# Performance work log

Measured on AMD Instinct MI355X. Metric: run time of the kernel, lower is better.

The kernel has to match this reference:

```python
import jax, jax.numpy as jnp
import numpy as np

N = 50000   # residue nodes
E = 800000  # edges per edge type
T = 3       # edge types
L = 3       # conv layers (len(hidden_channels)-1)
IN, H, ENC, OUT, K = 64, 128, 100, 32, 128
COMMIT = 0.25
EPS = 1e-5


def gelu(x):
    return jax.nn.gelu(x, approximate=False)  # torch nn.GELU default (erf)


def setup_inputs() -> dict:
    key = jax.random.key(0)
    ks = iter(jax.random.split(key, 40))
    p = lambda shp, s=0.05: jax.random.normal(next(ks), shp, jnp.float32) * s
    inp = {
        'x_res': p((N, IN), 1.0),
        'x_AA': p((N, 20), 1.0),
        'edge_index': jax.random.randint(next(ks), (T, 2, E), 0, N, jnp.int32),
        # input block
        'ln_gamma': jnp.ones((IN,), jnp.float32),
        'ln_beta': jnp.zeros((IN,), jnp.float32),
        'W1': p((IN, 2 * H)), 'b1': jnp.zeros((2 * H,), jnp.float32),
        'W2': p((2 * H, H)), 'b2': jnp.zeros((H,), jnp.float32),
        # body: SAGE convs, [layer, edge_type, ...]
        'sage_Wl': p((L, T, H, H)),  # applied to aggregated neighbors
        'sage_Wr': p((L, T, H, H)),  # applied to root
        'sage_b': jnp.zeros((L, T, H), jnp.float32),
        # GraphNorm per layer
        'gn_weight': jnp.ones((L, H), jnp.float32),
        'gn_bias': jnp.zeros((L, H), jnp.float32),
        'gn_scale': jnp.ones((L, H), jnp.float32),  # mean_scale
        # head
        'Wh1': p((H * L, ENC)), 'bh1': jnp.zeros((ENC,), jnp.float32),
        'Wh2': p((ENC, ENC)), 'bh2': jnp.zeros((ENC,), jnp.float32),
        'Wo1': p((ENC + 20, ENC)), 'bo1': jnp.zeros((ENC,), jnp.float32),
        'Wo2': p((ENC, ENC)), 'bo2': jnp.zeros((ENC,), jnp.float32),
        'Wo3': p((ENC, OUT)), 'bo3': jnp.zeros((OUT,), jnp.float32),
        # VQ codebook
        'codebook': p((K, OUT), 0.5),
    }
    return inp


def _sage(x, src, dst, Wl, Wr, b):
    # SAGEConv, mean aggregation: out = Wl @ mean_{src->dst}(x[src]) + Wr @ x + b
    msg = x[src]                                             # [E, H] gather
    s = jax.ops.segment_sum(msg, dst, num_segments=N)        # [N, H] scatter-add
    cnt = jax.ops.segment_sum(jnp.ones((msg.shape[0],), x.dtype), dst, num_segments=N)
    agg = s / jnp.maximum(cnt, 1.0)[:, None]
    return agg @ Wl + x @ Wr + b


def _graphnorm(x, weight, bias, scale):
    # PyG GraphNorm over a single graph
    out = x - scale * x.mean(0)
    var = (out * out).mean(0)
    return out * jax.lax.rsqrt(var + EPS) * weight + bias


def reference(x_res, x_AA, edge_index, ln_gamma, ln_beta, W1, b1, W2, b2,
              sage_Wl, sage_Wr, sage_b, gn_weight, gn_bias, gn_scale,
              Wh1, bh1, Wh2, bh2, Wo1, bo1, Wo2, bo2, Wo3, bo3, codebook):
    # input: LayerNorm + (dropout = identity in eval) + inmlp
    mu = x_res.mean(-1, keepdims=True)
    var = x_res.var(-1, keepdims=True)
    xr = (x_res - mu) * jax.lax.rsqrt(var + EPS) * ln_gamma + ln_beta
    x = gelu(gelu(xr @ W1 + b1) @ W2 + b2)                   # [N, H]

    # body: per-edge-type SAGE conv -> stack-mean -> GELU -> GraphNorm; JK cat
    x_save = []
    for i in range(L):
        xs = [_sage(x, edge_index[t, 0], edge_index[t, 1],
                    sage_Wl[i, t], sage_Wr[i, t], sage_b[i, t]) for t in range(T)]
        x = jnp.mean(jnp.stack(xs, 0), 0)
        x = gelu(x)
        x = _graphnorm(x, gn_weight[i], gn_bias[i], gn_scale[i])
        x_save.append(x)
    x = jnp.concatenate(x_save, axis=1)                      # [N, H*L] JumpingKnowledge cat

    # head
    x = gelu(gelu(x @ Wh1 + bh1) @ Wh2 + bh2)
    x = jnp.concatenate([x, x_AA], axis=1)
    x = gelu(x @ Wo1 + bo1)
    x = gelu(x @ Wo2 + bo2)
    x = jnp.tanh(x @ Wo3 + bo3)                              # [N, OUT]

    # VectorQuantizer (straight-through)
    d = (jnp.sum(x * x, 1, keepdims=True)
         - 2.0 * x @ codebook.T
         + jnp.sum(codebook * codebook, 1)[None, :])         # [N, K]
    idx = jnp.argmin(d, axis=1)
    q = codebook[idx]                                        # [N, OUT]
    e_latent = jnp.mean((jax.lax.stop_gradient(q) - x) ** 2)
    q_latent = jnp.mean((q - jax.lax.stop_gradient(x)) ** 2)
    vq_loss = q_latent + COMMIT * e_latent
    z_q = x + jax.lax.stop_gradient(q - x)
    return z_q, vq_loss
```

## Files before the change

### kernel.cpp

```cpp
#include <hip/hip_runtime.h>

#define N_ 50000
#define E_ 800000
#define T_ 3
#define NG_ (T_ * N_)
#define EPS_ 1e-5f

__device__ __forceinline__ float gelu_f(float x) {
    return 0.5f * x * (1.0f + erff(x * 0.70710678118654752440f));
}

__global__ void k_prep(const float* __restrict__ Wl, const float* __restrict__ Wr,
                       const float* __restrict__ b, float* wls, float* wra, float* ba) {
    int i = blockIdx.x * 256 + threadIdx.x;
    const float third = 1.0f / 3.0f;
    if (i < 9 * 128 * 128) wls[i] = Wl[i] * third;
    if (i < 3 * 128 * 128) {
        int l = i >> 14, rem = i & 16383;
        const float* p = Wr + l * 3 * 16384 + rem;
        wra[i] = (p[0] + p[16384] + p[32768]) * third;
    }
    if (i < 3 * 128) {
        int l = i >> 7, c = i & 127;
        const float* p = b + l * 3 * 128 + c;
        ba[i] = (p[0] + p[128] + p[256]) * third;
    }
}

__global__ void k_link(const int* __restrict__ EI, int* __restrict__ head, int* __restrict__ nxt) {
    int i = blockIdx.x * 256 + threadIdx.x;
    if (i >= T_ * E_) return;
    int t = i / E_, e = i - t * E_;
    int d = EI[(t * 2 + 1) * E_ + e];
    nxt[i] = atomicExch(&head[t * N_ + d], i);
}

__global__ __launch_bounds__(256) void k_compact(
    const int* __restrict__ EI, const int* __restrict__ head, const int* __restrict__ nxt,
    int* __restrict__ cursor, int* __restrict__ cnt, int* __restrict__ rpA,
    float* __restrict__ inv, int* __restrict__ csr) {
    int tid = threadIdx.x;
    int g = blockIdx.x * 256 + tid;
    bool ok = (g < NG_);
    int lane = tid & 63;
    int c = 0;
    int h = -1;
    if (ok) {
        h = head[g];
        int e = h;
        while (e >= 0) { c++; e = nxt[e]; }
        cnt[g] = c;
        inv[g] = 1.0f / (float)(c > 0 ? c : 1);
    }
    int x = c;
    for (int off = 1; off < 64; off <<= 1) {
        int y = __shfl_up(x, off);
        if (lane >= off) x += y;
    }
    int total = __shfl(x, 63);
    int base = 0;
    if (lane == 63 && total > 0) base = atomicAdd(cursor, total);
    base = __shfl(base, 63);
    if (ok) {
        int pos = base + x - c;
        rpA[g] = pos;
        int e = h;
        while (e >= 0) {
            int t = e / E_, idx = e - t * E_;
            csr[pos++] = EI[(t * 2) * E_ + idx];
            e = nxt[e];
        }
    }
}

__global__ __launch_bounds__(256) void k_inmlp(
    const float* __restrict__ xres, const float* __restrict__ gam, const float* __restrict__ bet,
    const float* __restrict__ W1, const float* __restrict__ b1,
    const float* __restrict__ W2, const float* __restrict__ b2, float* __restrict__ x0) {
    __shared__ float xr[32][68];
    __shared__ float h1[32][260];
    int tid = threadIdx.x;
    int base = blockIdx.x * 32;
    for (int i = 0; i < 2; ++i) {
        int f4 = i * 256 + tid;
        int r = f4 >> 4, c4 = f4 & 15;
        float4 v = make_float4(0.f, 0.f, 0.f, 0.f);
        int gr = base + r;
        if (gr < N_) v = *(const float4*)&xres[gr * 64 + c4 * 4];
        *(float4*)&xr[r][c4 * 4] = v;
    }
    __syncthreads();
    if (tid < 32) {
        int r = tid;
        float s = 0.f;
        for (int k = 0; k < 64; ++k) s += xr[r][k];
        float mu = s * (1.0f / 64.0f);
        float v = 0.f;
        for (int k = 0; k < 64; ++k) { float d = xr[r][k] - mu; v += d * d; }
        float rs = rsqrtf(v * (1.0f / 64.0f) + EPS_);
        for (int k = 0; k < 64; ++k)
            xr[r][k] = (xr[r][k] - mu) * rs * gam[k] + bet[k];
    }
    __syncthreads();
    {
        int tx = tid & 63, ty = tid >> 6;
        int c0 = tx * 4, r0 = ty * 8;
        float acc[8][4];
        for (int r = 0; r < 8; ++r)
            for (int j = 0; j < 4; ++j) acc[r][j] = b1[c0 + j];
        for (int k0 = 0; k0 < 64; k0 += 4) {
            float4 a[8], w[4];
            for (int r = 0; r < 8; ++r) a[r] = *(const float4*)&xr[r0 + r][k0];
            for (int kk = 0; kk < 4; ++kk) w[kk] = *(const float4*)&W1[(k0 + kk) * 256 + c0];
            for (int kk = 0; kk < 4; ++kk)
                for (int r = 0; r < 8; ++r) {
                    float as = (&a[r].x)[kk];
                    acc[r][0] = fmaf(as, w[kk].x, acc[r][0]);
                    acc[r][1] = fmaf(as, w[kk].y, acc[r][1]);
                    acc[r][2] = fmaf(as, w[kk].z, acc[r][2]);
                    acc[r][3] = fmaf(as, w[kk].w, acc[r][3]);
                }
        }
        for (int r = 0; r < 8; ++r)
            for (int j = 0; j < 4; ++j) h1[r0 + r][c0 + j] = gelu_f(acc[r][j]);
    }
    __syncthreads();
    {
        int tx = tid & 31, ty = tid >> 5;
        int c0 = tx * 4, r0 = ty * 4;
        float acc[4][4];
        for (int r = 0; r < 4; ++r)
            for (int j = 0; j < 4; ++j) acc[r][j] = b2[c0 + j];
        for (int k0 = 0; k0 < 256; k0 += 4) {
            float4 a[4], w[4];
            for (int r = 0; r < 4; ++r) a[r] = *(const float4*)&h1[r0 + r][k0];
            for (int kk = 0; kk < 4; ++kk) w[kk] = *(const float4*)&W2[(k0 + kk) * 128 + c0];
            for (int kk = 0; kk < 4; ++kk)
                for (int r = 0; r < 4; ++r) {
                    float as = (&a[r].x)[kk];
                    acc[r][0] = fmaf(as, w[kk].x, acc[r][0]);
                    acc[r][1] = fmaf(as, w[kk].y, acc[r][1]);
                    acc[r][2] = fmaf(as, w[kk].z, acc[r][2]);
                    acc[r][3] = fmaf(as, w[kk].w, acc[r][3]);
                }
        }
        for (int r = 0; r < 4; ++r) {
            int gr = base + r0 + r;
            if (gr < N_) {
                float4 v = make_float4(gelu_f(acc[r][0]), gelu_f(acc[r][1]),
                                       gelu_f(acc[r][2]), gelu_f(acc[r][3]));
                *(float4*)&x0[(long)gr * 128 + c0] = v;
            }
        }
    }
}

__global__ __launch_bounds__(256) void k_gather(
    const int* __restrict__ rpA, const int* __restrict__ cnt, const int* __restrict__ csr,
    const float* __restrict__ inv, const float* __restrict__ X, int ldx, float* __restrict__ agg) {
    int tid = threadIdx.x;
    int g = blockIdx.x * 4 + (tid >> 6);
    if (g >= NG_) return;
    int lane = tid & 63;
    int sub = lane >> 4;
    int f = (lane & 15) * 8;
    int start = rpA[g];
    int end = start + cnt[g];
    float4 s0 = make_float4(0.f, 0.f, 0.f, 0.f);
    float4 s1 = make_float4(0.f, 0.f, 0.f, 0.f);
    for (int e = start + sub; e < end; e += 4) {
        int sn = csr[e];
        const float* row = &X[(long)sn * ldx + f];
        const float4 v0 = *(const float4*)row;
        const float4 v1 = *(const float4*)(row + 4);
        s0.x += v0.x; s0.y += v0.y; s0.z += v0.z; s0.w += v0.w;
        s1.x += v1.x; s1.y += v1.y; s1.z += v1.z; s1.w += v1.w;
    }
    s0.x += __shfl_xor(s0.x, 16); s0.y += __shfl_xor(s0.y, 16);
    s0.z += __shfl_xor(s0.z, 16); s0.w += __shfl_xor(s0.w, 16);
    s1.x += __shfl_xor(s1.x, 16); s1.y += __shfl_xor(s1.y, 16);
    s1.z += __shfl_xor(s1.z, 16); s1.w += __shfl_xor(s1.w, 16);
    s0.x += __shfl_xor(s0.x, 32); s0.y += __shfl_xor(s0.y, 32);
    s0.z += __shfl_xor(s0.z, 32); s0.w += __shfl_xor(s0.w, 32);
    s1.x += __shfl_xor(s1.x, 32); s1.y += __shfl_xor(s1.y, 32);
    s1.z += __shfl_xor(s1.z, 32); s1.w += __shfl_xor(s1.w, 32);
    if (sub == 0) {
        float iv = inv[g];
        float* op = &agg[(long)g * 128 + f];
        *(float4*)op = make_float4(s0.x * iv, s0.y * iv, s0.z * iv, s0.w * iv);
        *(float4*)(op + 4) = make_float4(s1.x * iv, s1.y * iv, s1.z * iv, s1.w * iv);
    }
}

__global__ __launch_bounds__(256) void k_gemm_body(
    const float* __restrict__ X, int ldx, const float* __restrict__ agg,
    const float* __restrict__ wls_l, const float* __restrict__ wra_l, const float* __restrict__ ba_l,
    float* __restrict__ g_out, float* __restrict__ cs_l, float* __restrict__ cq_l) {
    __shared__ float xs[64][132];
    __shared__ float sd[8][128];
    __shared__ float sq[8][128];
    int tid = threadIdx.x;
    int base = blockIdx.x * 64;
    int tx = tid & 31, ty = tid >> 5;
    int c0 = tx * 4, r0 = ty * 8;
    float acc[8][4];
    for (int r = 0; r < 8; ++r)
        for (int j = 0; j < 4; ++j) acc[r][j] = ba_l[c0 + j];
    for (int seg = 0; seg < 4; ++seg) {
        const float* src; long ld;
        if (seg < 3) { src = agg + ((long)seg * N_ + base) * 128; ld = 128; }
        else         { src = X + (long)base * ldx; ld = ldx; }
        __syncthreads();
        for (int i = 0; i < 8; ++i) {
            int f4 = i * 256 + tid;
            int r = f4 >> 5, c4 = f4 & 31;
            float4 v = make_float4(0.f, 0.f, 0.f, 0.f);
            if (base + r < N_) v = *(const float4*)&src[(long)r * ld + c4 * 4];
            *(float4*)&xs[r][c4 * 4] = v;
        }
        __syncthreads();
        const float* W = (seg < 3) ? (wls_l + seg * 16384) : wra_l;
        for (int k0 = 0; k0 < 128; k0 += 4) {
            float4 a[8], w[4];
            for (int r = 0; r < 8; ++r) a[r] = *(const float4*)&xs[r0 + r][k0];
            for (int kk = 0; kk < 4; ++kk) w[kk] = *(const float4*)&W[(k0 + kk) * 128 + c0];
            for (int kk = 0; kk < 4; ++kk)
                for (int r = 0; r < 8; ++r) {
                    float as = (&a[r].x)[kk];
                    acc[r][0] = fmaf(as, w[kk].x, acc[r][0]);
                    acc[r][1] = fmaf(as, w[kk].y, acc[r][1]);
                    acc[r][2] = fmaf(as, w[kk].z, acc[r][2]);
                    acc[r][3] = fmaf(as, w[kk].w, acc[r][3]);
                }
        }
    }
    float csum[4] = {0.f, 0.f, 0.f, 0.f};
    float qsum[4] = {0.f, 0.f, 0.f, 0.f};
    for (int r = 0; r < 8; ++r) {
        int gr = base + r0 + r;
        if (gr < N_) {
            float g0 = gelu_f(acc[r][0]), g1 = gelu_f(acc[r][1]);
            float g2 = gelu_f(acc[r][2]), g3 = gelu_f(acc[r][3]);
            *(float4*)&g_out[(long)gr * 128 + c0] = make_float4(g0, g1, g2, g3);
            csum[0] += g0; csum[1] += g1; csum[2] += g2; csum[3] += g3;
            qsum[0] += g0 * g0; qsum[1] += g1 * g1; qsum[2] += g2 * g2; qsum[3] += g3 * g3;
        }
    }
    *(float4*)&sd[ty][c0] = make_float4(csum[0], csum[1], csum[2], csum[3]);
    *(float4*)&sq[ty][c0] = make_float4(qsum[0], qsum[1], qsum[2], qsum[3]);
    __syncthreads();
    if (tid < 128) {
        float t = 0.f, q = 0.f;
        for (int i = 0; i < 8; ++i) { t += sd[i][tid]; q += sq[i][tid]; }
        atomicAdd(&cs_l[tid], t);
        atomicAdd(&cq_l[tid], q);
    }
}

__global__ __launch_bounds__(256) void k_pass3(const float* __restrict__ g,
                                               const float* __restrict__ cs_l, const float* __restrict__ cq_l,
                                               const float* __restrict__ gsc,
                                               const float* __restrict__ gw, const float* __restrict__ gb,
                                               float* __restrict__ xs_l) {
    int tid = threadIdx.x;
    int c = tid & 127, half = tid >> 7;
    int base = blockIdx.x * 128 + half * 64;
    float mu = cs_l[c] / 50000.0f;
    float sm = gsc[c] * mu;
    float var = cq_l[c] / 50000.0f - 2.0f * sm * mu + sm * sm;
    float mul = rsqrtf(var + EPS_) * gw[c];
    float add = gb[c];
    for (int i = 0; i < 64; ++i) {
        int r = base + i;
        if (r < N_) xs_l[(long)r * 384 + c] = (g[(long)r * 128 + c] - sm) * mul + add;
    }
}

__global__ __launch_bounds__(256) void k_head1(const float* __restrict__ xsave,
    const float* __restrict__ Wh1, const float* __restrict__ bh1,
    const float* __restrict__ Wh2, const float* __restrict__ bh2,
    float* __restrict__ h2out) {
    __shared__ float at[64][68];
    __shared__ float h1b[64][104];
    int tid = threadIdx.x;
    int base = blockIdx.x * 64;
    int tx = tid & 31, ty = tid >> 5;
    int c0 = tx * 4, r0 = ty * 8;
    bool valid = (c0 < 100);
    float acc[8][4];
    for (int r = 0; r < 8; ++r)
        for (int j = 0; j < 4; ++j) acc[r][j] = valid ? bh1[c0 + j] : 0.f;
    for (int kt = 0; kt < 6; ++kt) {
        __syncthreads();
        for (int i = 0; i < 4; ++i) {
            int f4 = i * 256 + tid;
            int r = f4 >> 4, c4 = f4 & 15;
            float4 v = make_float4(0.f, 0.f, 0.f, 0.f);
            int gr = base + r;
            if (gr < N_) v = *(const float4*)&xsave[(long)gr * 384 + kt * 64 + c4 * 4];
            *(float4*)&at[r][c4 * 4] = v;
        }
        __syncthreads();
        if (valid) {
            for (int k0 = 0; k0 < 64; k0 += 4) {
                float4 a[8], w[4];
                for (int r = 0; r < 8; ++r) a[r] = *(const float4*)&at[r0 + r][k0];
                for (int kk = 0; kk < 4; ++kk) w[kk] = *(const float4*)&Wh1[(kt * 64 + k0 + kk) * 100 + c0];
                for (int kk = 0; kk < 4; ++kk)
                    for (int r = 0; r < 8; ++r) {
                        float as = (&a[r].x)[kk];
                        acc[r][0] = fmaf(as, w[kk].x, acc[r][0]);
                        acc[r][1] = fmaf(as, w[kk].y, acc[r][1]);
                        acc[r][2] = fmaf(as, w[kk].z, acc[r][2]);
                        acc[r][3] = fmaf(as, w[kk].w, acc[r][3]);
                    }
            }
        }
    }
    __syncthreads();
    if (valid)
        for (int r = 0; r < 8; ++r)
            for (int j = 0; j < 4; ++j) h1b[r0 + r][c0 + j] = gelu_f(acc[r][j]);
    __syncthreads();
    {
        float acc2[8][4];
        for (int r = 0; r < 8; ++r)
            for (int j = 0; j < 4; ++j) acc2[r][j] = valid ? bh2[c0 + j] : 0.f;
        if (valid) {
            for (int k0 = 0; k0 < 100; k0 += 4) {
                float4 a[8], w[4];
                for (int r = 0; r < 8; ++r) a[r] = *(const float4*)&h1b[r0 + r][k0];
                for (int kk = 0; kk < 4; ++kk) w[kk] = *(const float4*)&Wh2[(k0 + kk) * 100 + c0];
                for (int kk = 0; kk < 4; ++kk)
                    for (int r = 0; r < 8; ++r) {
                        float as = (&a[r].x)[kk];
                        acc2[r][0] = fmaf(as, w[kk].x, acc2[r][0]);
                        acc2[r][1] = fmaf(as, w[kk].y, acc2[r][1]);
                        acc2[r][2] = fmaf(as, w[kk].z, acc2[r][2]);
                        acc2[r][3] = fmaf(as, w[kk].w, acc2[r][3]);
                    }
            }
            for (int r = 0; r < 8; ++r) {
                int gr = base + r0 + r;
                if (gr < N_) {
                    float4 v = make_float4(gelu_f(acc2[r][0]), gelu_f(acc2[r][1]),
                                           gelu_f(acc2[r][2]), gelu_f(acc2[r][3]));
                    *(float4*)&h2out[(long)gr * 100 + c0] = v;
                }
            }
        }
    }
}

__global__ __launch_bounds__(256) void k_head2a(const float* __restrict__ h2,
    const float* __restrict__ xAA,
    const float* __restrict__ Wo1, const float* __restrict__ bo1,
    const float* __restrict__ Wo2, const float* __restrict__ bo2,
    const float* __restrict__ Wo3, const float* __restrict__ bo3,
    float* __restrict__ xf) {
    __shared__ float A[64][124];
    __shared__ float B[64][104];
    int tid = threadIdx.x;
    int base = blockIdx.x * 64;
    for (int i = 0; i < 7; ++i) {
        int f4 = i * 256 + tid;
        if (f4 < 1600) {
            int r = f4 / 25, c4 = f4 - r * 25;
            float4 v = make_float4(0.f, 0.f, 0.f, 0.f);
            int gr = base + r;
            if (gr < N_) v = *(const float4*)&h2[(long)gr * 100 + c4 * 4];
            *(float4*)&A[r][c4 * 4] = v;
        }
    }
    for (int i = 0; i < 2; ++i) {
        int f4 = i * 256 + tid;
        if (f4 < 320) {
            int r = f4 / 5, c4 = f4 - r * 5;
            float4 v = make_float4(0.f, 0.f, 0.f, 0.f);
            int gr = base + r;
            if (gr < N_) v = *(const float4*)&xAA[(long)gr * 20 + c4 * 4];
            *(float4*)&A[r][100 + c4 * 4] = v;
        }
    }
    __syncthreads();
    int tx = tid & 31, ty = tid >> 5;
    int c0 = tx * 4, r0 = ty * 8;
    bool valid = (c0 < 100);
    {
        float acc[8][4];
        for (int r = 0; r < 8; ++r)
            for (int j = 0; j < 4; ++j) acc[r][j] = valid ? bo1[c0 + j] : 0.f;
        if (valid) {
            for (int k0 = 0; k0 < 120; k0 += 4) {
                float4 a[8], w[4];
                for (int r = 0; r < 8; ++r) a[r] = *(const float4*)&A[r0 + r][k0];
                for (int kk = 0; kk < 4; ++kk) w[kk] = *(const float4*)&Wo1[(k0 + kk) * 100 + c0];
                for (int kk = 0; kk < 4; ++kk)
                    for (int r = 0; r < 8; ++r) {
                        float as = (&a[r].x)[kk];
                        acc[r][0] = fmaf(as, w[kk].x, acc[r][0]);
                        acc[r][1] = fmaf(as, w[kk].y, acc[r][1]);
                        acc[r][2] = fmaf(as, w[kk].z, acc[r][2]);
                        acc[r][3] = fmaf(as, w[kk].w, acc[r][3]);
                    }
            }
            for (int r = 0; r < 8; ++r)
                for (int j = 0; j < 4; ++j) B[r0 + r][c0 + j] = gelu_f(acc[r][j]);
        }
    }
    __syncthreads();
    {
        float acc[8][4];
        for (int r = 0; r < 8; ++r)
            for (int j = 0; j < 4; ++j) acc[r][j] = valid ? bo2[c0 + j] : 0.f;
        if (valid) {
            for (int k0 = 0; k0 < 100; k0 += 4) {
                float4 a[8], w[4];
                for (int r = 0; r < 8; ++r) a[r] = *(const float4*)&B[r0 + r][k0];
                for (int kk = 0; kk < 4; ++kk) w[kk] = *(const float4*)&Wo2[(k0 + kk) * 100 + c0];
                for (int kk = 0; kk < 4; ++kk)
                    for (int r = 0; r < 8; ++r) {
                        float as = (&a[r].x)[kk];
                        acc[r][0] = fmaf(as, w[kk].x, acc[r][0]);
                        acc[r][1] = fmaf(as, w[kk].y, acc[r][1]);
                        acc[r][2] = fmaf(as, w[kk].z, acc[r][2]);
                        acc[r][3] = fmaf(as, w[kk].w, acc[r][3]);
                    }
            }
        }
        __syncthreads();
        if (valid)
            for (int r = 0; r < 8; ++r)
                for (int j = 0; j < 4; ++j) A[r0 + r][c0 + j] = gelu_f(acc[r][j]);
    }
    __syncthreads();
    {
        int c0b = (tid & 7) * 4, rg = tid >> 3;
        int r0b = rg * 2;
        float acc[2][4];
        for (int r = 0; r < 2; ++r)
            for (int j = 0; j < 4; ++j) acc[r][j] = bo3[c0b + j];
        for (int k0 = 0; k0 < 100; k0 += 4) {
            float4 a[2], w[4];
            for (int r = 0; r < 2; ++r) a[r] = *(const float4*)&A[r0b + r][k0];
            for (int kk = 0; kk < 4; ++kk) w[kk] = *(const float4*)&Wo3[(k0 + kk) * 32 + c0b];
            for (int kk = 0; kk < 4; ++kk)
                for (int r = 0; r < 2; ++r) {
                    float as = (&a[r].x)[kk];
                    acc[r][0] = fmaf(as, w[kk].x, acc[r][0]);
                    acc[r][1] = fmaf(as, w[kk].y, acc[r][1]);
                    acc[r][2] = fmaf(as, w[kk].z, acc[r][2]);
                    acc[r][3] = fmaf(as, w[kk].w, acc[r][3]);
                }
        }
        for (int r = 0; r < 2; ++r) {
            int gr = base + r0b + r;
            if (gr < N_) {
                float4 v = make_float4(tanhf(acc[r][0]), tanhf(acc[r][1]),
                                       tanhf(acc[r][2]), tanhf(acc[r][3]));
                *(float4*)&xf[(long)gr * 32 + c0b] = v;
            }
        }
    }
}

__global__ __launch_bounds__(256) void k_vq(const float* __restrict__ xf,
    const float* __restrict__ cb, float* __restrict__ zq, float* __restrict__ loss) {
    __shared__ float CB[128 * 32];
    __shared__ float CC[128];
    __shared__ float SR[256];
    int tid = threadIdx.x;
    for (int i = 0; i < 4; ++i) {
        int f4 = i * 256 + tid;
        *(float4*)&CB[f4 * 4] = *(const float4*)&cb[f4 * 4];
    }
    __syncthreads();
    if (tid < 128) {
        float s = 0.f;
        for (int j = 0; j < 32; ++j) { float v = CB[tid * 32 + j]; s += v * v; }
        CC[tid] = s;
    }
    __syncthreads();
    int node = blockIdx.x * 256 + tid;
    float part = 0.f;
    if (node < N_) {
        float4 xv[8];
        for (int j4 = 0; j4 < 8; ++j4) xv[j4] = *(const float4*)&xf[(long)node * 32 + j4 * 4];
        float xx = 0.f;
        for (int j4 = 0; j4 < 8; ++j4)
            xx += xv[j4].x * xv[j4].x + xv[j4].y * xv[j4].y + xv[j4].z * xv[j4].z + xv[j4].w * xv[j4].w;
        float best = 3.4e38f;
        int bidx = 0;
        for (int k = 0; k < 128; ++k) {
            const float* cbr = &CB[k * 32];
            float dot = 0.f;
            for (int j4 = 0; j4 < 8; ++j4) {
                float4 cv = *(const float4*)&cbr[j4 * 4];
                dot += cv.x * xv[j4].x + cv.y * xv[j4].y + cv.z * xv[j4].z + cv.w * xv[j4].w;
            }
            float d = fmaf(-2.0f, dot, xx) + CC[k];
            if (d < best) { best = d; bidx = k; }
        }
        const float* q = &CB[bidx * 32];
        for (int j4 = 0; j4 < 8; ++j4) {
            float4 qv = *(const float4*)&q[j4 * 4];
            *(float4*)&zq[(long)node * 32 + j4 * 4] = qv;
            float4 xvv = xv[j4];
            float d0 = qv.x - xvv.x, d1 = qv.y - xvv.y, d2 = qv.z - xvv.z, d3 = qv.w - xvv.w;
            part += d0 * d0 + d1 * d1 + d2 * d2 + d3 * d3;
        }
    }
    SR[tid] = part;
    __syncthreads();
    for (int off = 128; off > 0; off >>= 1) {
        if (tid < off) SR[tid] += SR[tid + off];
        __syncthreads();
    }
    if (tid == 0) atomicAdd(loss, SR[0]);
}

__global__ void k_fin(float* dout, const float* loss) {
    if (threadIdx.x == 0 && blockIdx.x == 0)
        dout[(long)N_ * 32] = 1.25f * (loss[0] / 1600000.0f);
}

extern "C" void kernel_launch(void* const* d_in, const int* in_sizes, int n_in,
                              void* d_out, int out_size, void* d_ws, size_t ws_size,
                              hipStream_t stream) {
    const float* x_res = (const float*)d_in[0];
    const float* x_AA  = (const float*)d_in[1];
    const int*   EI    = (const int*)d_in[2];
    const float* ln_g  = (const float*)d_in[3];
    const float* ln_b  = (const float*)d_in[4];
    const float* W1    = (const float*)d_in[5];
    const float* b1    = (const float*)d_in[6];
    const float* W2    = (const float*)d_in[7];
    const float* b2    = (const float*)d_in[8];
    const float* sWl   = (const float*)d_in[9];
    const float* sWr   = (const float*)d_in[10];
    const float* sb    = (const float*)d_in[11];
    const float* gnw   = (const float*)d_in[12];
    const float* gnb   = (const float*)d_in[13];
    const float* gns   = (const float*)d_in[14];
    const float* Wh1   = (const float*)d_in[15];
    const float* bh1   = (const float*)d_in[16];
    const float* Wh2   = (const float*)d_in[17];
    const float* bh2   = (const float*)d_in[18];
    const float* Wo1   = (const float*)d_in[19];
    const float* bo1   = (const float*)d_in[20];
    const float* Wo2   = (const float*)d_in[21];
    const float* bo2   = (const float*)d_in[22];
    const float* Wo3   = (const float*)d_in[23];
    const float* bo3   = (const float*)d_in[24];
    const float* cbk   = (const float*)d_in[25];
    float* out = (float*)d_out;

    float* ws    = (float*)d_ws;
    float* xsave = ws;
    float* x0    = xsave + (size_t)N_ * 384;
    float* agg   = x0 + (size_t)N_ * 128;
    float* gbuf  = agg + (size_t)3 * N_ * 128;
    float* wls   = gbuf + (size_t)N_ * 128;
    float* wra   = wls + 147456;
    float* ba    = wra + 49152;
    int*   cursor = (int*)(ba + 384);
    float* loss  = (float*)(cursor + 1);
    float* cs    = loss + 1;
    float* cq    = cs + 384;
    int*   head  = (int*)(cq + 384);
    int*   nxt   = head + NG_;
    int*   cnt   = nxt + (size_t)T_ * E_;
    int*   rpA   = cnt + NG_;
    float* inv   = (float*)(rpA + NG_);
    int*   csr   = (int*)(inv + NG_);
    float* h2    = agg + (size_t)N_ * 128;
    float* xf    = gbuf;

    hipMemsetAsync(cursor, 0, 770 * sizeof(int), stream);
    hipMemsetAsync(head, 0xFF, NG_ * sizeof(int), stream);

    k_prep<<<576, 256, 0, stream>>>(sWl, sWr, sb, wls, wra, ba);
    k_link<<<(T_ * E_ + 255) / 256, 256, 0, stream>>>(EI, head, nxt);
    k_compact<<<(NG_ + 255) / 256, 256, 0, stream>>>(EI, head, nxt, cursor, cnt, rpA, inv, csr);
    k_inmlp<<<(N_ + 31) / 32, 256, 0, stream>>>(x_res, ln_g, ln_b, W1, b1, W2, b2, x0);

    for (int l = 0; l < 3; ++l) {
        const float* X = (l == 0) ? x0 : (xsave + (size_t)(l - 1) * 128);
        int ldx = (l == 0) ? 128 : 384;
        k_gather<<<NG_ / 4, 256, 0, stream>>>(rpA, cnt, csr, inv, X, ldx, agg);
        k_gemm_body<<<(N_ + 63) / 64, 256, 0, stream>>>(X, ldx, agg,
            wls + (size_t)l * 3 * 16384, wra + (size_t)l * 16384, ba + l * 128,
            gbuf, cs + l * 128, cq + l * 128);
        k_pass3<<<(N_ + 127) / 128, 256, 0, stream>>>(gbuf, cs + l * 128, cq + l * 128,
                                                      gns + l * 128, gnw + l * 128, gnb + l * 128,
                                                      xsave + (size_t)l * 128);
    }
    k_head1<<<(N_ + 63) / 64, 256, 0, stream>>>(xsave, Wh1, bh1, Wh2, bh2, h2);
    k_head2a<<<(N_ + 63) / 64, 256, 0, stream>>>(h2, x_AA, Wo1, bo1, Wo2, bo2, Wo3, bo3, xf);
    k_vq<<<(N_ + 255) / 256, 256, 0, stream>>>(xf, cbk, out, loss);
    k_fin<<<1, 64, 0, stream>>>(out, loss);
}
```

Measured before the change: 1.518 ms.

## Fold GraphNorm affine into consumers and fuse head kernels

GraphNorm is no longer applied in a separate pass over the activations. The body GEMM writes pre-norm GELU output directly into the JK buffer, a tiny kernel computes per-channel scale and shift, and the next layer's gather, root load and the head apply that affine on the fly. For the gather, the shift is added only when a node has at least one incoming edge, which keeps the mean aggregation correct. The two head kernels are merged into one so the h2 intermediate stays in shared memory, and the input LayerNorm statistics are parallelised across 8 lanes per row. This removes a full read/write pass of N×128 per layer plus an N×100 round trip, at the cost of a few extra FMAs per element in the gather.

```diff
diff --git a/kernel.cpp b/kernel.cpp
--- a/kernel.cpp
+++ b/kernel.cpp
@@ -11,7 +11,8 @@
 }
 
 __global__ void k_prep(const float* __restrict__ Wl, const float* __restrict__ Wr,
-                       const float* __restrict__ b, float* wls, float* wra, float* ba) {
+                       const float* __restrict__ b, float* wls, float* wra, float* ba,
+                       float* idA, float* idB) {
     int i = blockIdx.x * 256 + threadIdx.x;
     const float third = 1.0f / 3.0f;
     if (i < 9 * 128 * 128) wls[i] = Wl[i] * third;
@@ -25,6 +26,7 @@
         const float* p = b + l * 3 * 128 + c;
         ba[i] = (p[0] + p[128] + p[256]) * third;
     }
+    if (i < 128) { idA[i] = 1.0f; idB[i] = 0.0f; }
 }
 
 __global__ void k_link(const int* __restrict__ EI, int* __restrict__ head, int* __restrict__ nxt) {
@@ -90,15 +92,17 @@
         *(float4*)&xr[r][c4 * 4] = v;
     }
     __syncthreads();
-    if (tid < 32) {
-        int r = tid;
+    {
+        int r = tid >> 3, l8 = tid & 7;
         float s = 0.f;
-        for (int k = 0; k < 64; ++k) s += xr[r][k];
+        for (int k = l8; k < 64; k += 8) s += xr[r][k];
+        s += __shfl_xor(s, 1); s += __shfl_xor(s, 2); s += __shfl_xor(s, 4);
         float mu = s * (1.0f / 64.0f);
         float v = 0.f;
-        for (int k = 0; k < 64; ++k) { float d = xr[r][k] - mu; v += d * d; }
+        for (int k = l8; k < 64; k += 8) { float d = xr[r][k] - mu; v += d * d; }
+        v += __shfl_xor(v, 1); v += __shfl_xor(v, 2); v += __shfl_xor(v, 4);
         float rs = rsqrtf(v * (1.0f / 64.0f) + EPS_);
-        for (int k = 0; k < 64; ++k)
+        for (int k = l8; k < 64; k += 8)
             xr[r][k] = (xr[r][k] - mu) * rs * gam[k] + bet[k];
     }
     __syncthreads();
@@ -157,7 +161,8 @@
 
 __global__ __launch_bounds__(256) void k_gather(
     const int* __restrict__ rpA, const int* __restrict__ cnt, const int* __restrict__ csr,
-    const float* __restrict__ inv, const float* __restrict__ X, int ldx, float* __restrict__ agg) {
+    const float* __restrict__ inv, const float* __restrict__ X, int ldx,
+    const float* __restrict__ nA, const float* __restrict__ nB, float* __restrict__ agg) {
     int tid = threadIdx.x;
     int g = blockIdx.x * 4 + (tid >> 6);
     if (g >= NG_) return;
@@ -186,21 +191,35 @@
     s1.z += __shfl_xor(s1.z, 32); s1.w += __shfl_xor(s1.w, 32);
     if (sub == 0) {
         float iv = inv[g];
+        float bsel = (end > start) ? 1.0f : 0.0f;
+        float4 A0 = *(const float4*)&nA[f];
+        float4 A1 = *(const float4*)&nA[f + 4];
+        float4 B0 = *(const float4*)&nB[f];
+        float4 B1 = *(const float4*)&nB[f + 4];
         float* op = &agg[(long)g * 128 + f];
-        *(float4*)op = make_float4(s0.x * iv, s0.y * iv, s0.z * iv, s0.w * iv);
-        *(float4*)(op + 4) = make_float4(s1.x * iv, s1.y * iv, s1.z * iv, s1.w * iv);
+        *(float4*)op = make_float4(fmaf(s0.x * iv, A0.x, bsel * B0.x),
+                                   fmaf(s0.y * iv, A0.y, bsel * B0.y),
+                                   fmaf(s0.z * iv, A0.z, bsel * B0.z),
+                                   fmaf(s0.w * iv, A0.w, bsel * B0.w));
+        *(float4*)(op + 4) = make_float4(fmaf(s1.x * iv, A1.x, bsel * B1.x),
+                                         fmaf(s1.y * iv, A1.y, bsel * B1.y),
+                                         fmaf(s1.z * iv, A1.z, bsel * B1.z),
+                                         fmaf(s1.w * iv, A1.w, bsel * B1.w));
     }
 }
 
 __global__ __launch_bounds__(256) void k_gemm_body(
     const float* __restrict__ X, int ldx, const float* __restrict__ agg,
+    const float* __restrict__ nA, const float* __restrict__ nB,
     const float* __restrict__ wls_l, const float* __restrict__ wra_l, const float* __restrict__ ba_l,
-    float* __restrict__ g_out, float* __restrict__ cs_l, float* __restrict__ cq_l) {
+    float* __restrict__ xsl, float* __restrict__ cs_l, float* __restrict__ cq_l) {
     __shared__ float xs[64][132];
     __shared__ float sd[8][128];
     __shared__ float sq[8][128];
+    __shared__ float nAs[128], nBs[128];
     int tid = threadIdx.x;
     int base = blockIdx.x * 64;
+    if (tid < 128) { nAs[tid] = nA[tid]; nBs[tid] = nB[tid]; }
     int tx = tid & 31, ty = tid >> 5;
     int c0 = tx * 4, r0 = ty * 8;
     float acc[8][4];
@@ -216,6 +235,13 @@
             int r = f4 >> 5, c4 = f4 & 31;
             float4 v = make_float4(0.f, 0.f, 0.f, 0.f);
             if (base + r < N_) v = *(const float4*)&src[(long)r * ld + c4 * 4];
+            if (seg == 3) {
+                int cc = c4 * 4;
+                v.x = fmaf(v.x, nAs[cc], nBs[cc]);
+                v.y = fmaf(v.y, nAs[cc + 1], nBs[cc + 1]);
+                v.z = fmaf(v.z, nAs[cc + 2], nBs[cc + 2]);
+                v.w = fmaf(v.w, nAs[cc + 3], nBs[cc + 3]);
+            }
             *(float4*)&xs[r][c4 * 4] = v;
         }
         __syncthreads();
@@ -241,7 +267,7 @@
         if (gr < N_) {
             float g0 = gelu_f(acc[r][0]), g1 = gelu_f(acc[r][1]);
             float g2 = gelu_f(acc[r][2]), g3 = gelu_f(acc[r][3]);
-            *(float4*)&g_out[(long)gr * 128 + c0] = make_float4(g0, g1, g2, g3);
+            *(float4*)&xsl[(long)gr * 384 + c0] = make_float4(g0, g1, g2, g3);
             csum[0] += g0; csum[1] += g1; csum[2] += g2; csum[3] += g3;
             qsum[0] += g0 * g0; qsum[1] += g1 * g1; qsum[2] += g2 * g2; qsum[3] += g3 * g3;
         }
@@ -257,33 +283,33 @@
     }
 }
 
-__global__ __launch_bounds__(256) void k_pass3(const float* __restrict__ g,
-                                               const float* __restrict__ cs_l, const float* __restrict__ cq_l,
-                                               const float* __restrict__ gsc,
-                                               const float* __restrict__ gw, const float* __restrict__ gb,
-                                               float* __restrict__ xs_l) {
-    int tid = threadIdx.x;
-    int c = tid & 127, half = tid >> 7;
-    int base = blockIdx.x * 128 + half * 64;
+__global__ void k_norm(const float* __restrict__ cs_l, const float* __restrict__ cq_l,
+                       const float* __restrict__ gsc, const float* __restrict__ gw,
+                       const float* __restrict__ gb, float* __restrict__ nA, float* __restrict__ nB) {
+    int c = threadIdx.x;
     float mu = cs_l[c] / 50000.0f;
     float sm = gsc[c] * mu;
     float var = cq_l[c] / 50000.0f - 2.0f * sm * mu + sm * sm;
-    float mul = rsqrtf(var + EPS_) * gw[c];
-    float add = gb[c];
-    for (int i = 0; i < 64; ++i) {
-        int r = base + i;
-        if (r < N_) xs_l[(long)r * 384 + c] = (g[(long)r * 128 + c] - sm) * mul + add;
-    }
-}
-
-__global__ __launch_bounds__(256) void k_head1(const float* __restrict__ xsave,
+    float a = rsqrtf(var + EPS_) * gw[c];
+    nA[c] = a;
+    nB[c] = gb[c] - sm * a;
+}
+
+__global__ __launch_bounds__(256) void k_head(const float* __restrict__ xsave,
+    const float* __restrict__ nA, const float* __restrict__ nB,
     const float* __restrict__ Wh1, const float* __restrict__ bh1,
     const float* __restrict__ Wh2, const float* __restrict__ bh2,
-    float* __restrict__ h2out) {
-    __shared__ float at[64][68];
-    __shared__ float h1b[64][104];
+    const float* __restrict__ xAA,
+    const float* __restrict__ Wo1, const float* __restrict__ bo1,
+    const float* __restrict__ Wo2, const float* __restrict__ bo2,
+    const float* __restrict__ Wo3, const float* __restrict__ bo3,
+    float* __restrict__ xf) {
+    __shared__ __align__(16) float buf0[64 * 124];
+    __shared__ __align__(16) float buf1[64 * 104];
+    __shared__ float nAs[384], nBs[384];
     int tid = threadIdx.x;
     int base = blockIdx.x * 64;
+    for (int i = tid; i < 384; i += 256) { nAs[i] = nA[i]; nBs[i] = nB[i]; }
     int tx = tid & 31, ty = tid >> 5;
     int c0 = tx * 4, r0 = ty * 8;
     bool valid = (c0 < 100);
@@ -295,16 +321,21 @@
         for (int i = 0; i < 4; ++i) {
             int f4 = i * 256 + tid;
             int r = f4 >> 4, c4 = f4 & 15;
+            int col = kt * 64 + c4 * 4;
             float4 v = make_float4(0.f, 0.f, 0.f, 0.f);
             int gr = base + r;
-            if (gr < N_) v = *(const float4*)&xsave[(long)gr * 384 + kt * 64 + c4 * 4];
-            *(float4*)&at[r][c4 * 4] = v;
+            if (gr < N_) v = *(const float4*)&xsave[(long)gr * 384 + col];
+            v.x = fmaf(v.x, nAs[col], nBs[col]);
+            v.y = fmaf(v.y, nAs[col + 1], nBs[col + 1]);
+            v.z = fmaf(v.z, nAs[col + 2], nBs[col + 2]);
+            v.w = fmaf(v.w, nAs[col + 3], nBs[col + 3]);
+            *(float4*)&buf0[r * 68 + c4 * 4] = v;
         }
         __syncthreads();
         if (valid) {
             for (int k0 = 0; k0 < 64; k0 += 4) {
                 float4 a[8], w[4];
-                for (int r = 0; r < 8; ++r) a[r] = *(const float4*)&at[r0 + r][k0];
+                for (int r = 0; r < 8; ++r) a[r] = *(const float4*)&buf0[(r0 + r) * 68 + k0];
                 for (int kk = 0; kk < 4; ++kk) w[kk] = *(const float4*)&Wh1[(kt * 64 + k0 + kk) * 100 + c0];
                 for (int kk = 0; kk < 4; ++kk)
                     for (int r = 0; r < 8; ++r) {
@@ -320,8 +351,18 @@
     __syncthreads();
     if (valid)
         for (int r = 0; r < 8; ++r)
-            for (int j = 0; j < 4; ++j) h1b[r0 + r][c0 + j] = gelu_f(acc[r][j]);
-    __syncthreads();
+            for (int j = 0; j < 4; ++j) buf1[(r0 + r) * 104 + c0 + j] = gelu_f(acc[r][j]);
+    __syncthreads();
+    for (int i = 0; i < 2; ++i) {
+        int f4 = i * 256 + tid;
+        if (f4 < 320) {
+            int r = f4 / 5, c4 = f4 - r * 5;
+            float4 v = make_float4(0.f, 0.f, 0.f, 0.f);
+            int gr = base + r;
+            if (gr < N_) v = *(const float4*)&xAA[(long)gr * 20 + c4 * 4];
+            *(float4*)&buf0[r * 124 + 100 + c4 * 4] = v;
+        }
+    }
     {
         float acc2[8][4];
         for (int r = 0; r < 8; ++r)
@@ -329,7 +370,7 @@
         if (valid) {
             for (int k0 = 0; k0 < 100; k0 += 4) {
                 float4 a[8], w[4];
-                for (int r = 0; r < 8; ++r) a[r] = *(const float4*)&h1b[r0 + r][k0];
+                for (int r = 0; r < 8; ++r) a[r] = *(const float4*)&buf1[(r0 + r) * 104 + k0];
                 for (int kk = 0; kk < 4; ++kk) w[kk] = *(const float4*)&Wh2[(k0 + kk) * 100 + c0];
                 for (int kk = 0; kk < 4; ++kk)
                     for (int r = 0; r < 8; ++r) {
@@ -340,124 +381,85 @@
                         acc2[r][3] = fmaf(as, w[kk].w, acc2[r][3]);
                     }
             }
-            for (int r = 0; r < 8; ++r) {
-                int gr = base + r0 + r;
-                if (gr < N_) {
-                    float4 v = make_float4(gelu_f(acc2[r][0]), gelu_f(acc2[r][1]),
-                                           gelu_f(acc2[r][2]), gelu_f(acc2[r][3]));
-                    *(float4*)&h2out[(long)gr * 100 + c0] = v;
-                }
-            }
-        }
-    }
-}
-
-__global__ __launch_bounds__(256) void k_head2a(const float* __restrict__ h2,
-    const float* __restrict__ xAA,
-    const float* __restrict__ Wo1, const float* __restrict__ bo1,
-    const float* __restrict__ Wo2, const float* __restrict__ bo2,
-    const float* __restrict__ Wo3, const float* __restrict__ bo3,
-    float* __restrict__ xf) {
-    __shared__ float A[64][124];
-    __shared__ float B[64][104];
-    int tid = threadIdx.x;
-    int base = blockIdx.x * 64;
-    for (int i = 0; i < 7; ++i) {
-        int f4 = i * 256 + tid;
-        if (f4 < 1600) {
-            int r = f4 / 25, c4 = f4 - r * 25;
-            float4 v = make_float4(0.f, 0.f, 0.f, 0.f);
-            int gr = base + r;
-            if (gr < N_) v = *(const float4*)&h2[(long)gr * 100 + c4 * 4];
-            *(float4*)&A[r][c4 * 4] = v;
-        }
-    }
-    for (int i = 0; i < 2; ++i) {
-        int f4 = i * 256 + tid;
-        if (f4 < 320) {
-            int r = f4 / 5, c4 = f4 - r * 5;
-            float4 v = make_float4(0.f, 0.f, 0.f, 0.f);
-            int gr = base + r;
-            if (gr < N_) v = *(const float4*)&xAA[(long)gr * 20 + c4 * 4];
-            *(float4*)&A[r][100 + c4 * 4] = v;
-        }
-    }
-    __syncthreads();
-    int tx = tid & 31, ty = tid >> 5;
-    int c0 = tx * 4, r0 = ty * 8;
-    bool valid = (c0 < 100);
+            for (int r = 0; r < 8; ++r)
+                for (int j = 0; j < 4; ++j) buf0[(r0 + r) * 124 + c0 + j] = gelu_f(acc2[r][j]);
+        }
+    }
+    __syncthreads();
     {
-        float acc[8][4];
+        float acc3[8][4];
         for (int r = 0; r < 8; ++r)
-            for (int j = 0; j < 4; ++j) acc[r][j] = valid ? bo1[c0 + j] : 0.f;
+            for (int j = 0; j < 4; ++j) acc3[r][j] = valid ? bo1[c0 + j] : 0.f;
         if (valid) {
             for (int k0 = 0; k0 < 120; k0 += 4) {
                 float4 a[8], w[4];
-                for (int r = 0; r < 8; ++r) a[r] = *(const float4*)&A[r0 + r][k0];
+                for (int r = 0; r < 8; ++r) a[r] = *(const float4*)&buf0[(r0 + r) * 124 + k0];
                 for (int kk = 0; kk < 4; ++kk) w[kk] = *(const float4*)&Wo1[(k0 + kk) * 100 + c0];
                 for (int kk = 0; kk < 4; ++kk)
                     for (int r = 0; r < 8; ++r) {
                         float as = (&a[r].x)[kk];
-                        acc[r][0] = fmaf(as, w[kk].x, acc[r][0]);
-                        acc[r][1] = fmaf(as, w[kk].y, acc[r][1]);
-                        acc[r][2] = fmaf(as, w[kk].z, acc[r][2]);
-                        acc[r][3] = fmaf(as, w[kk].w, acc[r][3]);
+                        acc3[r][0] = fmaf(as, w[kk].x, acc3[r][0]);
+                        acc3[r][1] = fmaf(as, w[kk].y, acc3[r][1]);
+                        acc3[r][2] = fmaf(as, w[kk].z, acc3[r][2]);
+                        acc3[r][3] = fmaf(as, w[kk].w, acc3[r][3]);
                     }
             }
+        }
+        __syncthreads();
+        if (valid)
             for (int r = 0; r < 8; ++r)
-                for (int j = 0; j < 4; ++j) B[r0 + r][c0 + j] = gelu_f(acc[r][j]);
-        }
+                for (int j = 0; j < 4; ++j) buf1[(r0 + r) * 104 + c0 + j] = gelu_f(acc3[r][j]);
     }
     __syncthreads();
     {
-        float acc[8][4];
+        float acc4[8][4];
         for (int r = 0; r < 8; ++r)
-            for (int j = 0; j < 4; ++j) acc[r][j] = valid ? bo2[c0 + j] : 0.f;
+            for (int j = 0; j < 4; ++j) acc4[r][j] = valid ? bo2[c0 + j] : 0.f;
         if (valid) {
             for (int k0 = 0; k0 < 100; k0 += 4) {
                 float4 a[8], w[4];
-                for (int r = 0; r < 8; ++r) a[r] = *(const float4*)&B[r0 + r][k0];
+                for (int r = 0; r < 8; ++r) a[r] = *(const float4*)&buf1[(r0 + r) * 104 + k0];
                 for (int kk = 0; kk < 4; ++kk) w[kk] = *(const float4*)&Wo2[(k0 + kk) * 100 + c0];
                 for (int kk = 0; kk < 4; ++kk)
                     for (int r = 0; r < 8; ++r) {
                         float as = (&a[r].x)[kk];
-                        acc[r][0] = fmaf(as, w[kk].x, acc[r][0]);
-                        acc[r][1] = fmaf(as, w[kk].y, acc[r][1]);
-                        acc[r][2] = fmaf(as, w[kk].z, acc[r][2]);
-                        acc[r][3] = fmaf(as, w[kk].w, acc[r][3]);
+                        acc4[r][0] = fmaf(as, w[kk].x, acc4[r][0]);
+                        acc4[r][1] = fmaf(as, w[kk].y, acc4[r][1]);
+                        acc4[r][2] = fmaf(as, w[kk].z, acc4[r][2]);
+                        acc4[r][3] = fmaf(as, w[kk].w, acc4[r][3]);
                     }
             }
         }
         __syncthreads();
         if (valid)
             for (int r = 0; r < 8; ++r)
-                for (int j = 0; j < 4; ++j) A[r0 + r][c0 + j] = gelu_f(acc[r][j]);
+                for (int j = 0; j < 4; ++j) buf0[(r0 + r) * 124 + c0 + j] = gelu_f(acc4[r][j]);
     }
     __syncthreads();
     {
         int c0b = (tid & 7) * 4, rg = tid >> 3;
         int r0b = rg * 2;
-        float acc[2][4];
+        float acc5[2][4];
         for (int r = 0; r < 2; ++r)
-            for (int j = 0; j < 4; ++j) acc[r][j] = bo3[c0b + j];
+            for (int j = 0; j < 4; ++j) acc5[r][j] = bo3[c0b + j];
         for (int k0 = 0; k0 < 100; k0 += 4) {
             float4 a[2], w[4];
-            for (int r = 0; r < 2; ++r) a[r] = *(const float4*)&A[r0b + r][k0];
+            for (int r = 0; r < 2; ++r) a[r] = *(const float4*)&buf0[(r0b + r) * 124 + k0];
             for (int kk = 0; kk < 4; ++kk) w[kk] = *(const float4*)&Wo3[(k0 + kk) * 32 + c0b];
             for (int kk = 0; kk < 4; ++kk)
                 for (int r = 0; r < 2; ++r) {
                     float as = (&a[r].x)[kk];
-                    acc[r][0] = fmaf(as, w[kk].x, acc[r][0]);
-                    acc[r][1] = fmaf(as, w[kk].y, acc[r][1]);
-                    acc[r][2] = fmaf(as, w[kk].z, acc[r][2]);
-                    acc[r][3] = fmaf(as, w[kk].w, acc[r][3]);
+                    acc5[r][0] = fmaf(as, w[kk].x, acc5[r][0]);
+                    acc5[r][1] = fmaf(as, w[kk].y, acc5[r][1]);
+                    acc5[r][2] = fmaf(as, w[kk].z, acc5[r][2]);
+                    acc5[r][3] = fmaf(as, w[kk].w, acc5[r][3]);
                 }
         }
         for (int r = 0; r < 2; ++r) {
             int gr = base + r0b + r;
             if (gr < N_) {
-                float4 v = make_float4(tanhf(acc[r][0]), tanhf(acc[r][1]),
-                                       tanhf(acc[r][2]), tanhf(acc[r][3]));
+                float4 v = make_float4(tanhf(acc5[r][0]), tanhf(acc5[r][1]),
+                                       tanhf(acc5[r][2]), tanhf(acc5[r][3]));
                 *(float4*)&xf[(long)gr * 32 + c0b] = v;
             }
         }
@@ -559,11 +561,14 @@
     float* xsave = ws;
     float* x0    = xsave + (size_t)N_ * 384;
     float* agg   = x0 + (size_t)N_ * 128;
-    float* gbuf  = agg + (size_t)3 * N_ * 128;
-    float* wls   = gbuf + (size_t)N_ * 128;
+    float* wls   = agg + (size_t)3 * N_ * 128;
     float* wra   = wls + 147456;
     float* ba    = wra + 49152;
-    int*   cursor = (int*)(ba + 384);
+    float* idA   = ba + 384;
+    float* idB   = idA + 128;
+    float* normA = idB + 128;
+    float* normB = normA + 384;
+    int*   cursor = (int*)(normB + 384);
     float* loss  = (float*)(cursor + 1);
     float* cs    = loss + 1;
     float* cq    = cs + 384;
@@ -573,13 +578,12 @@
     int*   rpA   = cnt + NG_;
     float* inv   = (float*)(rpA + NG_);
     int*   csr   = (int*)(inv + NG_);
-    float* h2    = agg + (size_t)N_ * 128;
-    float* xf    = gbuf;
+    float* xf    = x0;
 
     hipMemsetAsync(cursor, 0, 770 * sizeof(int), stream);
     hipMemsetAsync(head, 0xFF, NG_ * sizeof(int), stream);
 
-    k_prep<<<576, 256, 0, stream>>>(sWl, sWr, sb, wls, wra, ba);
+    k_prep<<<576, 256, 0, stream>>>(sWl, sWr, sb, wls, wra, ba, idA, idB);
     k_link<<<(T_ * E_ + 255) / 256, 256, 0, stream>>>(EI, head, nxt);
     k_compact<<<(NG_ + 255) / 256, 256, 0, stream>>>(EI, head, nxt, cursor, cnt, rpA, inv, csr);
     k_inmlp<<<(N_ + 31) / 32, 256, 0, stream>>>(x_res, ln_g, ln_b, W1, b1, W2, b2, x0);
@@ -587,16 +591,18 @@
     for (int l = 0; l < 3; ++l) {
         const float* X = (l == 0) ? x0 : (xsave + (size_t)(l - 1) * 128);
         int ldx = (l == 0) ? 128 : 384;
-        k_gather<<<NG_ / 4, 256, 0, stream>>>(rpA, cnt, csr, inv, X, ldx, agg);
-        k_gemm_body<<<(N_ + 63) / 64, 256, 0, stream>>>(X, ldx, agg,
+        const float* nAl = (l == 0) ? idA : (normA + (size_t)(l - 1) * 128);
+        const float* nBl = (l == 0) ? idB : (normB + (size_t)(l - 1) * 128);
+        k_gather<<<NG_ / 4, 256, 0, stream>>>(rpA, cnt, csr, inv, X, ldx, nAl, nBl, agg);
+        k_gemm_body<<<(N_ + 63) / 64, 256, 0, stream>>>(X, ldx, agg, nAl, nBl,
             wls + (size_t)l * 3 * 16384, wra + (size_t)l * 16384, ba + l * 128,
-            gbuf, cs + l * 128, cq + l * 128);
-        k_pass3<<<(N_ + 127) / 128, 256, 0, stream>>>(gbuf, cs + l * 128, cq + l * 128,
-                                                      gns + l * 128, gnw + l * 128, gnb + l * 128,
-                                                      xsave + (size_t)l * 128);
-    }
-    k_head1<<<(N_ + 63) / 64, 256, 0, stream>>>(xsave, Wh1, bh1, Wh2, bh2, h2);
-    k_head2a<<<(N_ + 63) / 64, 256, 0, stream>>>(h2, x_AA, Wo1, bo1, Wo2, bo2, Wo3, bo3, xf);
+            xsave + (size_t)l * 128, cs + l * 128, cq + l * 128);
+        k_norm<<<1, 128, 0, stream>>>(cs + l * 128, cq + l * 128, gns + l * 128,
+                                      gnw + l * 128, gnb + l * 128,
+                                      normA + (size_t)l * 128, normB + (size_t)l * 128);
+    }
+    k_head<<<(N_ + 63) / 64, 256, 0, stream>>>(xsave, normA, normB, Wh1, bh1, Wh2, bh2,
+                                               x_AA, Wo1, bo1, Wo2, bo2, Wo3, bo3, xf);
     k_vq<<<(N_ + 255) / 256, 256, 0, stream>>>(xf, cbk, out, loss);
     k_fin<<<1, 64, 0, stream>>>(out, loss);
 }
```

Result: faster. 1.464 ms (-3.6%).
